# Kernel optimization log

Hardware: AMD Instinct MI355X
Metric: run time of the kernel (lower is better)

The kernel has to match this reference:

```python
import jax, jax.numpy as jnp
import numpy as np

B, N, C_IN = 32, 1024, 128
F0, F1, F2 = 64, 64, 64
OUT = 10
RATIOS = (0.8, 0.8)
EPS = 1e-5


def setup_inputs() -> dict:
    key = jax.random.key(0)
    ks = jax.random.split(key, 16)
    N_nodes = jax.random.randint(ks[0], (B,), N // 2, N + 1)
    mask = (jnp.arange(N)[None, :] < N_nodes[:, None]).astype(jnp.float32)
    x = jax.random.normal(ks[1], (B, N, C_IN), dtype=jnp.float32)
    # sparse-ish symmetric binary adjacency restricted to valid nodes
    A = (jax.random.uniform(ks[2], (B, N, N)) < 0.02).astype(jnp.float32)
    A = jnp.maximum(A, jnp.swapaxes(A, 1, 2))
    A = A * mask[:, :, None] * mask[:, None, :]
    def lin(k, fi, fo):
        b = 1.0 / np.sqrt(fi)
        kw, kb = jax.random.split(k)
        return (jax.random.uniform(kw, (fi, fo), minval=-b, maxval=b),
                jax.random.uniform(kb, (fo,), minval=-b, maxval=b))
    W0, b0 = lin(ks[3], C_IN, F0)
    W1, b1 = lin(ks[4], F0, F1)
    W2, b2 = lin(ks[5], F1, F2)
    bp0 = 1.0 / np.sqrt(F0)
    p0 = jax.random.uniform(ks[6], (F0, 1), minval=-bp0, maxval=bp0)
    bp1 = 1.0 / np.sqrt(F1)
    p1 = jax.random.uniform(ks[7], (F1, 1), minval=-bp1, maxval=bp1)
    Wfc, bfc = lin(ks[8], F2, OUT)
    return {"x": x, "A": A, "mask": mask, "N_nodes": N_nodes,
            "W0": W0, "b0": b0, "W1": W1, "b1": b1, "W2": W2, "b2": b2,
            "p0": p0, "p1": p1, "Wfc": Wfc, "bfc": bfc}


def _gconv(x, A, W, b):
    # Kipf-Welling normalized Laplacian conv, batched dense
    n = A.shape[1]
    A_hat = A + jnp.eye(n, dtype=A.dtype)[None]
    D = (jnp.sum(A_hat, axis=1) + EPS) ** -0.5  # [B,N]
    L = D[:, :, None] * A_hat * D[:, None, :]
    h = jnp.einsum('bnm,bmc->bnc', L, x) @ W + b
    return jax.nn.relu(h)


def _pool(x, A, mask, N_nodes, p, ratio):
    Bc, Nc, C = x.shape
    y = (x.reshape(Bc * Nc, C) @ p).reshape(Bc, Nc)
    y = y / jnp.sqrt(jnp.sum(p ** 2))
    N_remove = (N_nodes.astype(jnp.float32) * (1.0 - ratio)).astype(N_nodes.dtype)
    # remove the N_remove lowest-scoring valid nodes per graph
    y_eff = jnp.where(mask > 0, y, jnp.inf)
    ranks = jnp.argsort(jnp.argsort(y_eff, axis=1), axis=1)  # ascending rank
    new_mask = mask * (ranks >= N_remove[:, None]).astype(mask.dtype)
    x = x * jnp.tanh(y)[:, :, None] * new_mask[:, :, None]
    A = new_mask[:, :, None] * A * new_mask[:, None, :]
    return x, A, new_mask, N_nodes - N_remove


def reference(x, A, mask, N_nodes, W0, b0, W1, b1, W2, b2, p0, p1, Wfc, bfc):
    x = _gconv(x, A, W0, b0)
    x, A, mask, N_nodes = _pool(x, A, mask, N_nodes, p0, RATIOS[0])
    x = _gconv(x, A, W1, b1)
    x, A, mask, N_nodes = _pool(x, A, mask, N_nodes, p1, RATIOS[1])
    x = _gconv(x, A, W2, b2)
    x = jnp.max(x, axis=1)  # global max pool over nodes [B,F2]
    return x @ Wfc + bfc
```

## Files before the change

### kernel.cpp

```cpp
#include <hip/hip_runtime.h>
#include <cstdint>
#include <cstddef>

#define BB 32
#define NN 1024
#define CIN 128
#define FF 64
#define NOUT 10
#define CAP 128
#define EPSV 1e-5f

__global__ __launch_bounds__(256) void k_front(const float* __restrict__ A,
                                               const float* __restrict__ x,
                                               const float* __restrict__ W0,
                                               unsigned short* __restrict__ adj,
                                               int* __restrict__ cnt,
                                               float* __restrict__ c1,
                                               float* __restrict__ c2,
                                               float* __restrict__ T) {
    __shared__ __align__(16) float Wl[CIN * 64];
    int tid = threadIdx.x;
    if (blockIdx.x >= 8192) {
        int gid = blockIdx.x - 8192;
        int b = gid & 31;
        int cch = gid >> 5;
        int row0 = (b << 10) + cch * 16;
        for (int t = tid; t < CIN * 16; t += 256)
            ((float4*)Wl)[t] = ((const float4*)W0)[t];
        __syncthreads();
        int wave = tid >> 6, lane = tid & 63;
        int rsub = lane >> 4, f0 = (lane & 15) * 4;
        int r = row0 + wave * 4 + rsub;
        const float4* xr = (const float4*)(x + (size_t)r * CIN);
        float4 acc = {0.f, 0.f, 0.f, 0.f};
#pragma unroll 4
        for (int k4 = 0; k4 < CIN / 4; ++k4) {
            float4 xv = xr[k4];
            float4 w0 = *(const float4*)&Wl[(k4 * 4 + 0) * 64 + f0];
            float4 w1 = *(const float4*)&Wl[(k4 * 4 + 1) * 64 + f0];
            float4 w2 = *(const float4*)&Wl[(k4 * 4 + 2) * 64 + f0];
            float4 w3 = *(const float4*)&Wl[(k4 * 4 + 3) * 64 + f0];
            acc.x += xv.x * w0.x; acc.y += xv.x * w0.y; acc.z += xv.x * w0.z; acc.w += xv.x * w0.w;
            acc.x += xv.y * w1.x; acc.y += xv.y * w1.y; acc.z += xv.y * w1.z; acc.w += xv.y * w1.w;
            acc.x += xv.z * w2.x; acc.y += xv.z * w2.y; acc.z += xv.z * w2.z; acc.w += xv.z * w2.w;
            acc.x += xv.w * w3.x; acc.y += xv.w * w3.y; acc.z += xv.w * w3.z; acc.w += xv.w * w3.w;
        }
        *(float4*)&T[(size_t)r * 64 + f0] = acc;
    } else {
        int wave = tid >> 6;
        int lane = tid & 63;
        int r = blockIdx.x * 4 + wave;
        const float4* Arow = (const float4*)(A + (size_t)r * NN);
        float4 v0 = Arow[lane];
        float4 v1 = Arow[64 + lane];
        float4 v2 = Arow[128 + lane];
        float4 v3 = Arow[192 + lane];
        size_t base = (size_t)r * CAP;
        int c = 0;
        unsigned long long lt = (lane == 0) ? 0ULL : ((1ULL << lane) - 1ULL);
        float4 vv[4] = {v0, v1, v2, v3};
#pragma unroll
        for (int it = 0; it < 4; ++it) {
            float4 v = vv[it];
            int j0 = it * 256 + lane * 4;
            unsigned long long m0 = __ballot(v.x != 0.f);
            unsigned long long m1 = __ballot(v.y != 0.f);
            unsigned long long m2 = __ballot(v.z != 0.f);
            unsigned long long m3 = __ballot(v.w != 0.f);
            int before = __popcll(m0 & lt) + __popcll(m1 & lt) +
                         __popcll(m2 & lt) + __popcll(m3 & lt);
            int p = c + before;
            if (v.x != 0.f) { if (p < CAP) adj[base + p] = (unsigned short)(j0 + 0); ++p; }
            if (v.y != 0.f) { if (p < CAP) adj[base + p] = (unsigned short)(j0 + 1); ++p; }
            if (v.z != 0.f) { if (p < CAP) adj[base + p] = (unsigned short)(j0 + 2); ++p; }
            if (v.w != 0.f) { if (p < CAP) adj[base + p] = (unsigned short)(j0 + 3); ++p; }
            c += __popcll(m0) + __popcll(m1) + __popcll(m2) + __popcll(m3);
        }
        if (lane == 0) {
            cnt[r] = (c > CAP) ? CAP : c;
            float D = 1.0f / sqrtf((float)c + 1.0f + EPSV);
            c1[r] = D;
            c2[r] = D * D;
        }
    }
}

__global__ __launch_bounds__(256) void k_mid(const unsigned short* __restrict__ adj,
                                             const int* __restrict__ cnt,
                                             const float* __restrict__ nm,
                                             float* __restrict__ c1, float* __restrict__ c2,
                                             const float* __restrict__ Xin,
                                             const float* __restrict__ W,
                                             const float* __restrict__ y,
                                             float* __restrict__ T) {
    __shared__ __align__(16) float Wl[64 * 64];
    int tid = threadIdx.x;
    if (blockIdx.x >= 8192) {
        int gid = blockIdx.x - 8192;
        int b = gid & 31;
        int cch = gid >> 5;
        int row0 = (b << 10) + cch * 16;
        for (int t = tid; t < 64 * 16; t += 256)
            ((float4*)Wl)[t] = ((const float4*)W)[t];
        __syncthreads();
        int wave = tid >> 6, lane = tid & 63;
        int rsub = lane >> 4, f0 = (lane & 15) * 4;
        int r = row0 + wave * 4 + rsub;
        float sc = tanhf(y[r]) * nm[r];
        const float4* xr = (const float4*)(Xin + (size_t)r * 64);
        float4 acc = {0.f, 0.f, 0.f, 0.f};
#pragma unroll 4
        for (int k4 = 0; k4 < 16; ++k4) {
            float4 xv = xr[k4];
            float4 w0 = *(const float4*)&Wl[(k4 * 4 + 0) * 64 + f0];
            float4 w1 = *(const float4*)&Wl[(k4 * 4 + 1) * 64 + f0];
            float4 w2 = *(const float4*)&Wl[(k4 * 4 + 2) * 64 + f0];
            float4 w3 = *(const float4*)&Wl[(k4 * 4 + 3) * 64 + f0];
            acc.x += xv.x * w0.x; acc.y += xv.x * w0.y; acc.z += xv.x * w0.z; acc.w += xv.x * w0.w;
            acc.x += xv.y * w1.x; acc.y += xv.y * w1.y; acc.z += xv.y * w1.z; acc.w += xv.y * w1.w;
            acc.x += xv.z * w2.x; acc.y += xv.z * w2.y; acc.z += xv.z * w2.z; acc.w += xv.z * w2.w;
            acc.x += xv.w * w3.x; acc.y += xv.w * w3.y; acc.z += xv.w * w3.z; acc.w += xv.w * w3.w;
        }
        acc.x *= sc; acc.y *= sc; acc.z *= sc; acc.w *= sc;
        *(float4*)&T[(size_t)r * 64 + f0] = acc;
    } else {
        int wave = tid >> 6, lane = tid & 63;
        int r = blockIdx.x * 4 + wave;
        int b = r >> 10;
        const unsigned short* arow = adj + (size_t)r * CAP;
        const float* nmb = nm + (b << 10);
        int n = cnt[r];
        float s = 0.f;
        if (lane < n)      s  = nmb[arow[lane]];
        if (lane + 64 < n) s += nmb[arow[lane + 64]];
        for (int sh = 32; sh; sh >>= 1) s += __shfl_xor(s, sh, 64);
        if (lane == 0) {
            float m = nm[r];
            float D = 1.0f / sqrtf(m * s + 1.0f + EPSV);
            c1[r] = m * D;
            c2[r] = D * D;
        }
    }
}

__global__ __launch_bounds__(256) void k_spmm(const unsigned short* __restrict__ adj,
                                              const int* __restrict__ cnt,
                                              const float* __restrict__ c1,
                                              const float* __restrict__ c2,
                                              const float* __restrict__ T,
                                              const float* __restrict__ bias,
                                              float* __restrict__ X,
                                              const float* __restrict__ p,
                                              float* __restrict__ y) {
    __shared__ __align__(16) float c1s[NN];
    int b   = blockIdx.x & 31;
    int cch = blockIdx.x >> 5;
    int tid = threadIdx.x;
    ((float4*)c1s)[tid] = ((const float4*)(c1 + (b << 10)))[tid];
    __syncthreads();
    int wave = tid >> 6, lane = tid & 63;
    int r = (b << 10) + cch * 4 + wave;
    const unsigned short* arow = adj + (size_t)r * CAP;
    int n = cnt[r];
    const float* Tb = T + ((size_t)(b << 10) << 6);
    float acc0 = 0.f, acc1 = 0.f, acc2 = 0.f, acc3 = 0.f;
    int t = 0;
    for (; t + 4 <= n; t += 4) {
        ushort4 j4 = *(const ushort4*)(arow + t);
        acc0 += c1s[j4.x] * Tb[((int)j4.x << 6) + lane];
        acc1 += c1s[j4.y] * Tb[((int)j4.y << 6) + lane];
        acc2 += c1s[j4.z] * Tb[((int)j4.z << 6) + lane];
        acc3 += c1s[j4.w] * Tb[((int)j4.w << 6) + lane];
    }
    for (; t < n; ++t) {
        int j = arow[t];
        acc0 += c1s[j] * Tb[(j << 6) + lane];
    }
    float acc = (acc0 + acc1) + (acc2 + acc3);
    int rl = r & 1023;
    float o = c1s[rl] * acc + c2[r] * T[((size_t)r << 6) + lane] + bias[lane];
    o = fmaxf(o, 0.f);
    X[((size_t)r << 6) + lane] = o;
    if (p != nullptr) {
        float pv = p[lane];
        float a = o * pv;
        float pp = pv * pv;
        for (int s = 32; s; s >>= 1) {
            a += __shfl_xor(a, s, 64);
            pp += __shfl_xor(pp, s, 64);
        }
        if (lane == 0) y[r] = a / sqrtf(pp);
    }
}

__global__ __launch_bounds__(256) void k_rank(const float* __restrict__ y,
                                              const float* __restrict__ maskSrc,
                                              const int* __restrict__ nsrc,
                                              float* __restrict__ nmOut,
                                              int* __restrict__ ncur) {
    __shared__ __align__(16) float yv[NN];
    int b = blockIdx.x >> 4;
    int sub = blockIdx.x & 15;
    int tid = threadIdx.x;
    const float INF = __builtin_inff();
    {
        float4 v = ((const float4*)(y + (b << 10)))[tid];
        float4 m = ((const float4*)(maskSrc + (b << 10)))[tid];
        v.x = (m.x > 0.f) ? v.x : INF;
        v.y = (m.y > 0.f) ? v.y : INF;
        v.z = (m.z > 0.f) ? v.z : INF;
        v.w = (m.w > 0.f) ? v.w : INF;
        ((float4*)yv)[tid] = v;
    }
    int n = nsrc[b];
    const float RM = (float)(1.0 - 0.8);
    int nrem = (int)((float)n * RM);
    if (sub == 0 && tid == 0) ncur[b] = n - nrem;
    __syncthreads();
    int i = (sub << 6) + (tid >> 2);
    int q = tid & 3;
    float yi = yv[i];
    int rank = 0;
    if (yi < INF) {
        const float4* jbase = (const float4*)yv + (q << 6);
        int j0 = q << 8;
#pragma unroll 8
        for (int t = 0; t < 64; ++t) {
            float4 a = jbase[t];
            int j = j0 + t * 4;
            rank += (a.x < yi || (a.x == yi && j     < i)) ? 1 : 0;
            rank += (a.y < yi || (a.y == yi && j + 1 < i)) ? 1 : 0;
            rank += (a.z < yi || (a.z == yi && j + 2 < i)) ? 1 : 0;
            rank += (a.w < yi || (a.w == yi && j + 3 < i)) ? 1 : 0;
        }
    }
    rank += __shfl_xor(rank, 1, 64);
    rank += __shfl_xor(rank, 2, 64);
    if (q == 0) {
        float nmv = (yi < INF && rank >= nrem) ? 1.f : 0.f;
        nmOut[(b << 10) + i] = nmv;
    }
}

__global__ __launch_bounds__(256) void k_final(const float* __restrict__ X,
                                               const float* __restrict__ Wfc,
                                               const float* __restrict__ bfc,
                                               float* __restrict__ out) {
    __shared__ float red[4][64];
    __shared__ float gl[64];
    int b = blockIdx.x, tid = threadIdx.x;
    int f = tid & 63, c = tid >> 6;
    float m = 0.f;
    for (int i = c; i < NN; i += 4)
        m = fmaxf(m, X[(((size_t)(b << 10) + i) << 6) + f]);
    red[c][f] = m;
    __syncthreads();
    if (tid < 64)
        gl[tid] = fmaxf(fmaxf(red[0][tid], red[1][tid]), fmaxf(red[2][tid], red[3][tid]));
    __syncthreads();
    if (tid < NOUT) {
        float acc = bfc[tid];
        for (int k = 0; k < 64; ++k) acc += gl[k] * Wfc[k * NOUT + tid];
        out[b * NOUT + tid] = acc;
    }
}

extern "C" void kernel_launch(void* const* d_in, const int* in_sizes, int n_in,
                              void* d_out, int out_size, void* d_ws, size_t ws_size,
                              hipStream_t stream) {
    const float* x    = (const float*)d_in[0];
    const float* A    = (const float*)d_in[1];
    const float* mask = (const float*)d_in[2];
    const int*   Nn   = (const int*)d_in[3];
    const float* W0   = (const float*)d_in[4];
    const float* b0   = (const float*)d_in[5];
    const float* W1   = (const float*)d_in[6];
    const float* b1   = (const float*)d_in[7];
    const float* W2   = (const float*)d_in[8];
    const float* b2   = (const float*)d_in[9];
    const float* p0   = (const float*)d_in[10];
    const float* p1   = (const float*)d_in[11];
    const float* Wfc  = (const float*)d_in[12];
    const float* bfc  = (const float*)d_in[13];
    float* out = (float*)d_out;

    char* ws = (char*)d_ws;
    size_t off = 0;
    auto alloc = [&](size_t bytes) -> void* {
        void* p = ws + off;
        off = (off + bytes + 255) & ~(size_t)255;
        return p;
    };
    unsigned short* adj = (unsigned short*)alloc((size_t)BB * NN * CAP * 2);
    int*   cnt  = (int*)  alloc((size_t)BB * NN * 4);
    float* X    = (float*)alloc((size_t)BB * NN * 64 * 4);
    float* T    = (float*)alloc((size_t)BB * NN * 64 * 4);
    float* c1   = (float*)alloc((size_t)BB * NN * 4);
    float* c2   = (float*)alloc((size_t)BB * NN * 4);
    float* y    = (float*)alloc((size_t)BB * NN * 4);
    float* nm0  = (float*)alloc((size_t)BB * NN * 4);
    float* nm1  = (float*)alloc((size_t)BB * NN * 4);
    int*   nc0  = (int*)  alloc((size_t)BB * 4);
    int*   nc1  = (int*)  alloc((size_t)BB * 4);

    const int RW = BB * NN;
    k_front<<<8192 + 2048, 256, 0, stream>>>(A, x, W0, adj, cnt, c1, c2, T);
    k_spmm<<<RW / 4, 256, 0, stream>>>(adj, cnt, c1, c2, T, b0, X, p0, y);
    k_rank<<<BB * 16, 256, 0, stream>>>(y, mask, Nn, nm0, nc0);
    k_mid<<<8192 + 2048, 256, 0, stream>>>(adj, cnt, nm0, c1, c2, X, W1, y, T);
    k_spmm<<<RW / 4, 256, 0, stream>>>(adj, cnt, c1, c2, T, b1, X, p1, y);
    k_rank<<<BB * 16, 256, 0, stream>>>(y, nm0, nc0, nm1, nc1);
    k_mid<<<8192 + 2048, 256, 0, stream>>>(adj, cnt, nm1, c1, c2, X, W2, y, T);
    k_spmm<<<RW / 4, 256, 0, stream>>>(adj, cnt, c1, c2, T, b2, X, nullptr, nullptr);
    k_final<<<BB, 256, 0, stream>>>(X, Wfc, bfc, out);
}
```

Baseline: 376.3 us.

## Fuse global max pool into last SpMM, stage adjacency in LDS, 4 rows per wave

The last SpMM layer now skips writing X and folds the per-graph global max into a block reduction plus atomicMax. A small FC kernel then reads only the pooled vector, which removes a full pass over X. The adjacency compaction in k_front stages indices in shared memory and writes them to global as coalesced 32-bit words instead of scattered 16-bit stores. SpMM blocks now handle 16 rows each, with 4 rows per wave, so c1 is staged once per 16 rows and the norm of p is computed once per wave; this costs an extra memset and atomics.

```diff
diff --git a/kernel.cpp b/kernel.cpp
--- a/kernel.cpp
+++ b/kernel.cpp
@@ -20,6 +20,7 @@
                                                float* __restrict__ T) {
     __shared__ __align__(16) float Wl[CIN * 64];
     int tid = threadIdx.x;
+    int wave = tid >> 6, lane = tid & 63;
     if (blockIdx.x >= 8192) {
         int gid = blockIdx.x - 8192;
         int b = gid & 31;
@@ -28,7 +29,6 @@
         for (int t = tid; t < CIN * 16; t += 256)
             ((float4*)Wl)[t] = ((const float4*)W0)[t];
         __syncthreads();
-        int wave = tid >> 6, lane = tid & 63;
         int rsub = lane >> 4, f0 = (lane & 15) * 4;
         int r = row0 + wave * 4 + rsub;
         const float4* xr = (const float4*)(x + (size_t)r * CIN);
@@ -47,15 +47,13 @@
         }
         *(float4*)&T[(size_t)r * 64 + f0] = acc;
     } else {
-        int wave = tid >> 6;
-        int lane = tid & 63;
+        unsigned short* adjs = ((unsigned short*)Wl) + wave * CAP;
         int r = blockIdx.x * 4 + wave;
         const float4* Arow = (const float4*)(A + (size_t)r * NN);
         float4 v0 = Arow[lane];
         float4 v1 = Arow[64 + lane];
         float4 v2 = Arow[128 + lane];
         float4 v3 = Arow[192 + lane];
-        size_t base = (size_t)r * CAP;
         int c = 0;
         unsigned long long lt = (lane == 0) ? 0ULL : ((1ULL << lane) - 1ULL);
         float4 vv[4] = {v0, v1, v2, v3};
@@ -70,14 +68,17 @@
             int before = __popcll(m0 & lt) + __popcll(m1 & lt) +
                          __popcll(m2 & lt) + __popcll(m3 & lt);
             int p = c + before;
-            if (v.x != 0.f) { if (p < CAP) adj[base + p] = (unsigned short)(j0 + 0); ++p; }
-            if (v.y != 0.f) { if (p < CAP) adj[base + p] = (unsigned short)(j0 + 1); ++p; }
-            if (v.z != 0.f) { if (p < CAP) adj[base + p] = (unsigned short)(j0 + 2); ++p; }
-            if (v.w != 0.f) { if (p < CAP) adj[base + p] = (unsigned short)(j0 + 3); ++p; }
+            if (v.x != 0.f) { if (p < CAP) adjs[p] = (unsigned short)(j0 + 0); ++p; }
+            if (v.y != 0.f) { if (p < CAP) adjs[p] = (unsigned short)(j0 + 1); ++p; }
+            if (v.z != 0.f) { if (p < CAP) adjs[p] = (unsigned short)(j0 + 2); ++p; }
+            if (v.w != 0.f) { if (p < CAP) adjs[p] = (unsigned short)(j0 + 3); ++p; }
             c += __popcll(m0) + __popcll(m1) + __popcll(m2) + __popcll(m3);
         }
+        int cc = (c > CAP) ? CAP : c;
+        uint32_t* dst = (uint32_t*)(adj + (size_t)r * CAP);
+        if (lane * 2 < cc) dst[lane] = ((const uint32_t*)adjs)[lane];
         if (lane == 0) {
-            cnt[r] = (c > CAP) ? CAP : c;
+            cnt[r] = cc;
             float D = 1.0f / sqrtf((float)c + 1.0f + EPSV);
             c1[r] = D;
             c2[r] = D * D;
@@ -151,45 +152,65 @@
                                               const float* __restrict__ bias,
                                               float* __restrict__ X,
                                               const float* __restrict__ p,
-                                              float* __restrict__ y) {
+                                              float* __restrict__ y,
+                                              float* __restrict__ gmax) {
     __shared__ __align__(16) float c1s[NN];
+    __shared__ float red[4][64];
     int b   = blockIdx.x & 31;
     int cch = blockIdx.x >> 5;
     int tid = threadIdx.x;
     ((float4*)c1s)[tid] = ((const float4*)(c1 + (b << 10)))[tid];
     __syncthreads();
     int wave = tid >> 6, lane = tid & 63;
-    int r = (b << 10) + cch * 4 + wave;
-    const unsigned short* arow = adj + (size_t)r * CAP;
-    int n = cnt[r];
+    int r0 = (b << 10) + cch * 16 + wave * 4;
     const float* Tb = T + ((size_t)(b << 10) << 6);
-    float acc0 = 0.f, acc1 = 0.f, acc2 = 0.f, acc3 = 0.f;
-    int t = 0;
-    for (; t + 4 <= n; t += 4) {
-        ushort4 j4 = *(const ushort4*)(arow + t);
-        acc0 += c1s[j4.x] * Tb[((int)j4.x << 6) + lane];
-        acc1 += c1s[j4.y] * Tb[((int)j4.y << 6) + lane];
-        acc2 += c1s[j4.z] * Tb[((int)j4.z << 6) + lane];
-        acc3 += c1s[j4.w] * Tb[((int)j4.w << 6) + lane];
-    }
-    for (; t < n; ++t) {
-        int j = arow[t];
-        acc0 += c1s[j] * Tb[(j << 6) + lane];
-    }
-    float acc = (acc0 + acc1) + (acc2 + acc3);
-    int rl = r & 1023;
-    float o = c1s[rl] * acc + c2[r] * T[((size_t)r << 6) + lane] + bias[lane];
-    o = fmaxf(o, 0.f);
-    X[((size_t)r << 6) + lane] = o;
+    float bv = bias[lane];
+    float pv = 0.f, ppinv = 0.f;
     if (p != nullptr) {
-        float pv = p[lane];
-        float a = o * pv;
+        pv = p[lane];
         float pp = pv * pv;
-        for (int s = 32; s; s >>= 1) {
-            a += __shfl_xor(a, s, 64);
-            pp += __shfl_xor(pp, s, 64);
-        }
-        if (lane == 0) y[r] = a / sqrtf(pp);
+        for (int s = 32; s; s >>= 1) pp += __shfl_xor(pp, s, 64);
+        ppinv = 1.0f / sqrtf(pp);
+    }
+    float vmax = 0.f;
+#pragma unroll
+    for (int rr = 0; rr < 4; ++rr) {
+        int r = r0 + rr;
+        const unsigned short* arow = adj + (size_t)r * CAP;
+        int n = cnt[r];
+        float acc0 = 0.f, acc1 = 0.f, acc2 = 0.f, acc3 = 0.f;
+        int t = 0;
+        for (; t + 4 <= n; t += 4) {
+            ushort4 j4 = *(const ushort4*)(arow + t);
+            acc0 += c1s[j4.x] * Tb[((int)j4.x << 6) + lane];
+            acc1 += c1s[j4.y] * Tb[((int)j4.y << 6) + lane];
+            acc2 += c1s[j4.z] * Tb[((int)j4.z << 6) + lane];
+            acc3 += c1s[j4.w] * Tb[((int)j4.w << 6) + lane];
+        }
+        for (; t < n; ++t) {
+            int j = arow[t];
+            acc0 += c1s[j] * Tb[(j << 6) + lane];
+        }
+        float acc = (acc0 + acc1) + (acc2 + acc3);
+        int rl = r & 1023;
+        float o = c1s[rl] * acc + c2[r] * T[((size_t)r << 6) + lane] + bv;
+        o = fmaxf(o, 0.f);
+        if (X != nullptr) X[((size_t)r << 6) + lane] = o;
+        if (p != nullptr) {
+            float a = o * pv;
+            for (int s = 32; s; s >>= 1) a += __shfl_xor(a, s, 64);
+            if (lane == 0) y[r] = a * ppinv;
+        }
+        vmax = fmaxf(vmax, o);
+    }
+    if (gmax != nullptr) {
+        red[wave][lane] = vmax;
+        __syncthreads();
+        if (wave == 0) {
+            float m = fmaxf(fmaxf(red[0][lane], red[1][lane]),
+                            fmaxf(red[2][lane], red[3][lane]));
+            atomicMax((int*)&gmax[(b << 6) + lane], __float_as_int(m));
+        }
     }
 }
 
@@ -242,26 +263,18 @@
     }
 }
 
-__global__ __launch_bounds__(256) void k_final(const float* __restrict__ X,
-                                               const float* __restrict__ Wfc,
-                                               const float* __restrict__ bfc,
-                                               float* __restrict__ out) {
-    __shared__ float red[4][64];
+__global__ __launch_bounds__(64) void k_fc(const float* __restrict__ gmax,
+                                           const float* __restrict__ Wfc,
+                                           const float* __restrict__ bfc,
+                                           float* __restrict__ out) {
     __shared__ float gl[64];
-    int b = blockIdx.x, tid = threadIdx.x;
-    int f = tid & 63, c = tid >> 6;
-    float m = 0.f;
-    for (int i = c; i < NN; i += 4)
-        m = fmaxf(m, X[(((size_t)(b << 10) + i) << 6) + f]);
-    red[c][f] = m;
+    int b = blockIdx.x, lane = threadIdx.x;
+    gl[lane] = gmax[(b << 6) + lane];
     __syncthreads();
-    if (tid < 64)
-        gl[tid] = fmaxf(fmaxf(red[0][tid], red[1][tid]), fmaxf(red[2][tid], red[3][tid]));
-    __syncthreads();
-    if (tid < NOUT) {
-        float acc = bfc[tid];
-        for (int k = 0; k < 64; ++k) acc += gl[k] * Wfc[k * NOUT + tid];
-        out[b * NOUT + tid] = acc;
+    if (lane < NOUT) {
+        float acc = bfc[lane];
+        for (int k = 0; k < 64; ++k) acc += gl[k] * Wfc[k * NOUT + lane];
+        out[b * NOUT + lane] = acc;
     }
 }
 
@@ -302,15 +315,17 @@
     float* nm1  = (float*)alloc((size_t)BB * NN * 4);
     int*   nc0  = (int*)  alloc((size_t)BB * 4);
     int*   nc1  = (int*)  alloc((size_t)BB * 4);
+    float* gmax = (float*)alloc((size_t)BB * 64 * 4);
 
     const int RW = BB * NN;
+    hipMemsetAsync(gmax, 0, (size_t)BB * 64 * 4, stream);
     k_front<<<8192 + 2048, 256, 0, stream>>>(A, x, W0, adj, cnt, c1, c2, T);
-    k_spmm<<<RW / 4, 256, 0, stream>>>(adj, cnt, c1, c2, T, b0, X, p0, y);
+    k_spmm<<<2048, 256, 0, stream>>>(adj, cnt, c1, c2, T, b0, X, p0, y, nullptr);
     k_rank<<<BB * 16, 256, 0, stream>>>(y, mask, Nn, nm0, nc0);
     k_mid<<<8192 + 2048, 256, 0, stream>>>(adj, cnt, nm0, c1, c2, X, W1, y, T);
-    k_spmm<<<RW / 4, 256, 0, stream>>>(adj, cnt, c1, c2, T, b1, X, p1, y);
+    k_spmm<<<2048, 256, 0, stream>>>(adj, cnt, c1, c2, T, b1, X, p1, y, nullptr);
     k_rank<<<BB * 16, 256, 0, stream>>>(y, nm0, nc0, nm1, nc1);
     k_mid<<<8192 + 2048, 256, 0, stream>>>(adj, cnt, nm1, c1, c2, X, W2, y, T);
-    k_spmm<<<RW / 4, 256, 0, stream>>>(adj, cnt, c1, c2, T, b2, X, nullptr, nullptr);
-    k_final<<<BB, 256, 0, stream>>>(X, Wfc, bfc, out);
-}
+    k_spmm<<<2048, 256, 0, stream>>>(adj, cnt, c1, c2, T, b2, nullptr, nullptr, nullptr, gmax);
+    k_fc<<<BB, 64, 0, stream>>>(gmax, Wfc, bfc, out);
+}
```

Result: no change. 373.8 us (-0.6%).
